# Performance work log

Measured on AMD Instinct MI355X. Metric: run time of the kernel, lower is better.

## Reference

```python
import jax, jax.numpy as jnp
import numpy as np

SIZE = (128, 160, 128)  # (D, H, W)
BATCH, CHANNELS = 4, 1


def setup_inputs() -> dict:
    key = jax.random.key(0)
    k1, k2 = jax.random.split(key)
    src = jax.random.normal(k1, (BATCH, CHANNELS) + SIZE, dtype=jnp.float32)
    # near-identity affine [B, 3, 4] so most sampled coords land in-volume
    eye = jnp.concatenate([jnp.eye(3, dtype=jnp.float32), jnp.zeros((3, 1), jnp.float32)], axis=1)
    affine_matrix = eye[None] + 0.05 * jax.random.normal(k2, (BATCH, 3, 4), dtype=jnp.float32)
    return {"src": src, "affine_matrix": affine_matrix}


def _mesh_matrix(D, H, W):
    # rows: dim0 (D), dim1 (H), dim2 (W), ones  -> [4, N]
    gz, gy, gx = jnp.meshgrid(jnp.arange(D), jnp.arange(H), jnp.arange(W), indexing='ij')
    N = D * H * W
    return jnp.stack([gz.reshape(N), gy.reshape(N), gx.reshape(N),
                      jnp.ones((N,), jnp.int32)], axis=0).astype(jnp.float32)


def _trilinear_border(src, ix, iy, iz):
    # src: [B, C, D, H, W]; ix/iy/iz: [B, N] unnormalized pixel coords (x->W, y->H, z->D)
    B, C, D, H, W = src.shape
    # border padding: clamp coordinate before interpolation (matches PyTorch)
    ix = jnp.clip(ix, 0.0, W - 1.0)
    iy = jnp.clip(iy, 0.0, H - 1.0)
    iz = jnp.clip(iz, 0.0, D - 1.0)
    x0f, y0f, z0f = jnp.floor(ix), jnp.floor(iy), jnp.floor(iz)
    wx = (ix - x0f)[:, None, :]  # [B,1,N]
    wy = (iy - y0f)[:, None, :]
    wz = (iz - z0f)[:, None, :]
    x0 = x0f.astype(jnp.int32); x1 = jnp.minimum(x0 + 1, W - 1)
    y0 = y0f.astype(jnp.int32); y1 = jnp.minimum(y0 + 1, H - 1)
    z0 = z0f.astype(jnp.int32); z1 = jnp.minimum(z0 + 1, D - 1)
    flat = src.reshape(B, C, D * H * W)
    N = ix.shape[-1]

    def gather(zz, yy, xx):
        idx = (zz * H + yy) * W + xx  # [B, N]
        idx = jnp.broadcast_to(idx[:, None, :], (B, C, N))
        return jnp.take_along_axis(flat, idx, axis=2)  # [B, C, N]

    c000 = gather(z0, y0, x0); c001 = gather(z0, y0, x1)
    c010 = gather(z0, y1, x0); c011 = gather(z0, y1, x1)
    c100 = gather(z1, y0, x0); c101 = gather(z1, y0, x1)
    c110 = gather(z1, y1, x0); c111 = gather(z1, y1, x1)
    c00 = c000 + (c001 - c000) * wx
    c01 = c010 + (c011 - c010) * wx
    c10 = c100 + (c101 - c100) * wx
    c11 = c110 + (c111 - c110) * wx
    c0 = c00 + (c01 - c00) * wy
    c1 = c10 + (c11 - c10) * wy
    return c0 + (c1 - c0) * wz  # [B, C, N]


def reference(src, affine_matrix):
    D, H, W = SIZE
    B, C = src.shape[:2]
    mesh = _mesh_matrix(D, H, W)  # [4, N]
    loc = jnp.einsum('bij,jn->bin', affine_matrix, mesh)  # [B, 3, N] voxel coords
    sizes = jnp.array([D, H, W], jnp.float32)
    g = 2.0 * (loc / (sizes[None, :, None] - 1.0) - 0.5)  # normalized, dims (d0,d1,d2)
    # flip to grid_sample (x, y, z) ordering, then unnormalize (align_corners=False)
    ix = ((g[:, 2] + 1.0) * W - 1.0) * 0.5
    iy = ((g[:, 1] + 1.0) * H - 1.0) * 0.5
    iz = ((g[:, 0] + 1.0) * D - 1.0) * 0.5
    out = _trilinear_border(src, ix, iy, iz)  # [B, C, N]
    return out.reshape(B, C, D, H, W)
```

## Files before the change

kernel.cpp:

```cpp
#include <hip/hip_runtime.h>

#define DD 128
#define HH 160
#define WW 128
#define BB 4
#define HW  20480
#define DHW 2621440

#define TX 32
#define TY 8
#define TZ 8
#define XT 4
#define YT 20
#define ZT 16
#define NWG (XT * YT * ZT * BB)
#define NXCD 8
#define CPX (NWG / NXCD)

#define FZE   14
#define FYE   14
#define PITCH 44
#define SLABF (FYE * PITCH)
#define ROWB  (PITCH * 4)
#define SLABB (SLABF * 4)
#define NIT 9
#define LDSALLOC (NIT * 1024)

typedef float f2 __attribute__((ext_vector_type(2), aligned(4)));
typedef float v2 __attribute__((ext_vector_type(2)));

__global__ __launch_bounds__(256)
void st_affine_kernel(const float* __restrict__ src,
                      const float* __restrict__ aff,
                      float* __restrict__ out) {
    __shared__ float lds[LDSALLOC];

    const int wgid = blockIdx.x;
    const int lin  = (wgid & (NXCD - 1)) * CPX + (wgid >> 3);
    const int xt = lin & 3;
    const int l2 = lin >> 2;
    const int yt = l2 % YT;
    const int l3 = l2 / YT;
    const int zt = l3 & (ZT - 1);
    const int b  = l3 >> 4;
    const int x0t = xt * TX, y0t = yt * TY, z0t = zt * TZ;

    const float* A = aff + b * 12;
    const float cD = 128.f/127.f, cH = 160.f/159.f, cW = 128.f/127.f;
    const float pz0 = A[0]*cD, pz1 = A[1]*cD, pz2 = A[2]*cD,  pz3 = fmaf(A[3],  cD, -0.5f);
    const float py0 = A[4]*cH, py1 = A[5]*cH, py2 = A[6]*cH,  py3 = fmaf(A[7],  cH, -0.5f);
    const float px0 = A[8]*cW, px1 = A[9]*cW, px2 = A[10]*cW, px3 = fmaf(A[11], cW, -0.5f);

    const float hz = (TZ - 1) * 0.5f, hy = (TY - 1) * 0.5f, hx = (TX - 1) * 0.5f;
    const float ccz = (float)z0t + hz, ccy = (float)y0t + hy, ccx = (float)x0t + hx;
    const float izcn = fmaf(pz0, ccz, fmaf(pz1, ccy, fmaf(pz2, ccx, pz3)));
    const float iycn = fmaf(py0, ccz, fmaf(py1, ccy, fmaf(py2, ccx, py3)));
    const float ixcn = fmaf(px0, ccz, fmaf(px1, ccy, fmaf(px2, ccx, px3)));
    const float rz = fmaf(fabsf(pz0), hz, fmaf(fabsf(pz1), hy, fmaf(fabsf(pz2), hx, 1e-3f)));
    const float ry = fmaf(fabsf(py0), hz, fmaf(fabsf(py1), hy, fmaf(fabsf(py2), hx, 1e-3f)));
    const float rx = fmaf(fabsf(px0), hz, fmaf(fabsf(px1), hy, fmaf(fabsf(px2), hx, 1e-3f)));
    const float mnz = izcn - rz, mxz = izcn + rz;
    const float mny = iycn - ry, mxy = iycn + ry;
    const float mnx = ixcn - rx, mxx = ixcn + rx;

    const bool interior =
        (mnz > 0.02f) && (mxz < 126.98f) &&
        (mny > 0.02f) && (mxy < 158.98f) &&
        (mnx > 0.02f) && (mxx < 126.98f);

    const int xlo = max(0, (int)floorf(__builtin_amdgcn_fmed3f(mnx, 0.f, 127.f)) - 1);
    const int ylo = max(0, (int)floorf(__builtin_amdgcn_fmed3f(mny, 0.f, 159.f)) - 1);
    const int zlo = max(0, (int)floorf(__builtin_amdgcn_fmed3f(mnz, 0.f, 127.f)) - 1);
    const int xhi = min(WW - 2, (int)floorf(__builtin_amdgcn_fmed3f(mxx, 0.f, 127.f)) + 1);
    const int yhi = min(HH - 2, (int)floorf(__builtin_amdgcn_fmed3f(mxy, 0.f, 159.f)) + 1);
    const int zhi = min(DD - 2, (int)floorf(__builtin_amdgcn_fmed3f(mxz, 0.f, 127.f)) + 1);

    const int xlo4 = xlo & ~3;
    const int XE4  = xhi - xlo4 + 2;
    const int YE   = yhi - ylo + 2;
    const int ZE   = zhi - zlo + 2;
    const bool fits = (XE4 <= PITCH) && (YE <= FYE) && (ZE <= FZE);

    const float zloF = (float)zlo, yloF = (float)ylo, xlo4F = (float)xlo4;

    const int tid  = threadIdx.x;
    const int lane = tid & 63;
    const int wid  = tid >> 6;

    const int xq = x0t + (lane & 31);
    const int yo = y0t + (lane >> 5) + (wid << 1);
    const float fx0 = (float)xq, fy = (float)yo, fzb = (float)z0t;

    const float izb0 = fmaf(pz0, fzb, fmaf(pz1, fy, fmaf(pz2, fx0, pz3)));
    const float iyb0 = fmaf(py0, fzb, fmaf(py1, fy, fmaf(py2, fx0, py3)));
    const float ixb0 = fmaf(px0, fzb, fmaf(px1, fy, fmaf(px2, fx0, px3)));

    const float* sb = src + b * DHW;
    float* dst0 = out + (size_t)(((b * DD + z0t) * HH + yo) * WW + xq);

    if (fits) {
        const float RC154 = 1.f / 154.f, RC11 = 1.f / 11.f;
        const float gbase = fmaf(zloF, 20480.f, fmaf(yloF, 128.f, xlo4F));
        const int totalCh = ZE * FYE * 11;
        const int nIt = (totalCh + 255) >> 8;
        for (int it = 0; it < nIt; ++it) {
            const int k = (it << 8) + tid;
            float kf  = (float)k;
            float zif = floorf(fmaf(kf, RC154, 0.5f * RC154));
            float rem = fmaf(zif, -154.f, kf);
            float yif = floorf(fmaf(rem, RC11, 0.5f * RC11));
            float xif = fmaf(yif, -11.f, rem);
            float gf  = fmaf(zif, 20480.f, fmaf(yif, 128.f, fmaf(xif, 4.f, gbase)));
            int g = min((int)gf, DHW - 4);
            __builtin_amdgcn_global_load_lds(
                (const __attribute__((address_space(1))) void*)(sb + g),
                (__attribute__((address_space(3))) void*)(lds + (size_t)(((it << 8) + (wid << 6)) * 4)),
                16, 0, 0);
        }
    }
    __syncthreads();

    const char* Lb = (const char*)lds;

    auto triL = [&](int o0, int o1, v2 wx, v2 wy, v2 wz) -> v2 {
        f2 a00 = *(const f2*)(Lb + o0);
        f2 a01 = *(const f2*)(Lb + o0 + ROWB);
        f2 a10 = *(const f2*)(Lb + o0 + SLABB);
        f2 a11 = *(const f2*)(Lb + o0 + SLABB + ROWB);
        f2 b00 = *(const f2*)(Lb + o1);
        f2 b01 = *(const f2*)(Lb + o1 + ROWB);
        f2 b10 = *(const f2*)(Lb + o1 + SLABB);
        f2 b11 = *(const f2*)(Lb + o1 + SLABB + ROWB);
        v2 c00 = {fmaf(a00.y - a00.x, wx.x, a00.x), fmaf(b00.y - b00.x, wx.y, b00.x)};
        v2 c01 = {fmaf(a01.y - a01.x, wx.x, a01.x), fmaf(b01.y - b01.x, wx.y, b01.x)};
        v2 c10 = {fmaf(a10.y - a10.x, wx.x, a10.x), fmaf(b10.y - b10.x, wx.y, b10.x)};
        v2 c11 = {fmaf(a11.y - a11.x, wx.x, a11.x), fmaf(b11.y - b11.x, wx.y, b11.x)};
        v2 c0 = c00 + (c01 - c00) * wy;
        v2 c1 = c10 + (c11 - c10) * wy;
        return c0 + (c1 - c0) * wz;
    };

    if (fits) {
        const v2 dzv = {2.f * pz0, 2.f * pz0};
        const v2 dyv = {2.f * py0, 2.f * py0};
        const v2 dxv = {2.f * px0, 2.f * px0};
        const float hiZ = 127.f - zloF, capZ = 126.f - zloF;
        const float hiY = 159.f - yloF, capY = 158.f - yloF;
        const float hiX = 127.f - xlo4F, capX = 126.f - xlo4F;

        v2 az = {izb0 - zloF, izb0 + pz0 - zloF};
        v2 ay = {iyb0 - yloF, iyb0 + py0 - yloF};
        v2 ax = {ixb0 - xlo4F, ixb0 + px0 - xlo4F};

#pragma unroll
        for (int s = 0; s < 4; ++s) {
            v2 cz, cy, cx, wz, wy, wx;
            if (interior) {
                cz = v2{floorf(az.x), floorf(az.y)};
                cy = v2{floorf(ay.x), floorf(ay.y)};
                cx = v2{floorf(ax.x), floorf(ax.y)};
                wz = az - cz; wy = ay - cy; wx = ax - cx;
            } else {
                v2 azc = {__builtin_amdgcn_fmed3f(az.x, 0.f, hiZ),
                          __builtin_amdgcn_fmed3f(az.y, 0.f, hiZ)};
                v2 ayc = {__builtin_amdgcn_fmed3f(ay.x, 0.f, hiY),
                          __builtin_amdgcn_fmed3f(ay.y, 0.f, hiY)};
                v2 axc = {__builtin_amdgcn_fmed3f(ax.x, 0.f, hiX),
                          __builtin_amdgcn_fmed3f(ax.y, 0.f, hiX)};
                cz = v2{fminf(floorf(azc.x), capZ), fminf(floorf(azc.y), capZ)};
                cy = v2{fminf(floorf(ayc.x), capY), fminf(floorf(ayc.y), capY)};
                cx = v2{fminf(floorf(axc.x), capX), fminf(floorf(axc.y), capX)};
                wz = azc - cz; wy = ayc - cy; wx = axc - cx;
            }
            v2 ob = (cz * (float)FYE + cy) * (float)ROWB + cx * 4.f;
            v2 r = triL((int)ob.x, (int)ob.y, wx, wy, wz);
            float* d = dst0 + (s << 1) * HW;
            __builtin_nontemporal_store(r.x, d);
            __builtin_nontemporal_store(r.y, d + HW);
            az += dzv; ay += dyv; ax += dxv;
        }
    } else {
        v2 az = {izb0, izb0 + pz0};
        v2 ay = {iyb0, iyb0 + py0};
        v2 ax = {ixb0, ixb0 + px0};
        const v2 dzv = {2.f * pz0, 2.f * pz0};
        const v2 dyv = {2.f * py0, 2.f * py0};
        const v2 dxv = {2.f * px0, 2.f * px0};
#pragma unroll
        for (int s = 0; s < 4; ++s) {
            v2 azc = {__builtin_amdgcn_fmed3f(az.x, 0.f, 127.f),
                      __builtin_amdgcn_fmed3f(az.y, 0.f, 127.f)};
            v2 ayc = {__builtin_amdgcn_fmed3f(ay.x, 0.f, 159.f),
                      __builtin_amdgcn_fmed3f(ay.y, 0.f, 159.f)};
            v2 axc = {__builtin_amdgcn_fmed3f(ax.x, 0.f, 127.f),
                      __builtin_amdgcn_fmed3f(ax.y, 0.f, 127.f)};
            v2 cz = {fminf(floorf(azc.x), 126.f), fminf(floorf(azc.y), 126.f)};
            v2 cy = {fminf(floorf(ayc.x), 158.f), fminf(floorf(ayc.y), 158.f)};
            v2 cx = {fminf(floorf(axc.x), 126.f), fminf(floorf(axc.y), 126.f)};
            v2 wz = azc - cz, wy = ayc - cy, wx = axc - cx;
            auto g1 = [&](float czs, float cys, float cxs, float wxs, float wys, float wzs) -> float {
                int o = (int)fmaf(czs, 20480.f, fmaf(cys, 128.f, cxs));
                const float* p = sb + o;
                f2 v00 = *(const f2*)(p);
                f2 v01 = *(const f2*)(p + WW);
                f2 v10 = *(const f2*)(p + HW);
                f2 v11 = *(const f2*)(p + HW + WW);
                float c00 = fmaf(v00.y - v00.x, wxs, v00.x);
                float c01 = fmaf(v01.y - v01.x, wxs, v01.x);
                float c10 = fmaf(v10.y - v10.x, wxs, v10.x);
                float c11 = fmaf(v11.y - v11.x, wxs, v11.x);
                float c0 = fmaf(c01 - c00, wys, c00);
                float c1 = fmaf(c11 - c10, wys, c10);
                return fmaf(c1 - c0, wzs, c0);
            };
            float* d = dst0 + (s << 1) * HW;
            __builtin_nontemporal_store(g1(cz.x, cy.x, cx.x, wx.x, wy.x, wz.x), d);
            __builtin_nontemporal_store(g1(cz.y, cy.y, cx.y, wx.y, wy.y, wz.y), d + HW);
            az += dzv; ay += dyv; ax += dxv;
        }
    }
}

extern "C" void kernel_launch(void* const* d_in, const int* in_sizes, int n_in,
                              void* d_out, int out_size, void* d_ws, size_t ws_size,
                              hipStream_t stream) {
    const float* src = (const float*)d_in[0];
    const float* aff = (const float*)d_in[1];
    float* out = (float*)d_out;

    st_affine_kernel<<<dim3(NWG), dim3(256), 0, stream>>>(src, aff, out);
}
```

Before: 24.94 us.

## Enlarge workgroup tile in y and tighten the LDS staging box

Changes the output tile per workgroup from 32x8x8 to 32x16x8, so each thread handles two y-rows eight apart across all eight z-slices instead of two z-slices at a time. The LDS footprint grows in y to 21 rows and the slab chunk count is adjusted to match. The conservative -1/+1 margins on the source bounding box are dropped, which shrinks the region loaded into LDS. The aim is to cut redundant halo loads relative to useful output, at the cost of more LDS per workgroup (lower occupancy), half as many workgroups, and a higher chance that tiles fall back to the slower direct-global path.

```diff
diff --git a/kernel.cpp b/kernel.cpp
--- a/kernel.cpp
+++ b/kernel.cpp
@@ -8,23 +8,22 @@
 #define DHW 2621440
 
 #define TX 32
-#define TY 8
+#define TY 16
 #define TZ 8
 #define XT 4
-#define YT 20
+#define YT 10
 #define ZT 16
 #define NWG (XT * YT * ZT * BB)
 #define NXCD 8
 #define CPX (NWG / NXCD)
 
 #define FZE   14
-#define FYE   14
+#define FYE   21
 #define PITCH 44
-#define SLABF (FYE * PITCH)
 #define ROWB  (PITCH * 4)
-#define SLABB (SLABF * 4)
-#define NIT 9
-#define LDSALLOC (NIT * 1024)
+#define SLABB (FYE * ROWB)
+#define SLABCH (FYE * 11)
+#define LDSALLOC 13312
 
 typedef float f2 __attribute__((ext_vector_type(2), aligned(4)));
 typedef float v2 __attribute__((ext_vector_type(2)));
@@ -68,12 +67,12 @@
         (mny > 0.02f) && (mxy < 158.98f) &&
         (mnx > 0.02f) && (mxx < 126.98f);
 
-    const int xlo = max(0, (int)floorf(__builtin_amdgcn_fmed3f(mnx, 0.f, 127.f)) - 1);
-    const int ylo = max(0, (int)floorf(__builtin_amdgcn_fmed3f(mny, 0.f, 159.f)) - 1);
-    const int zlo = max(0, (int)floorf(__builtin_amdgcn_fmed3f(mnz, 0.f, 127.f)) - 1);
-    const int xhi = min(WW - 2, (int)floorf(__builtin_amdgcn_fmed3f(mxx, 0.f, 127.f)) + 1);
-    const int yhi = min(HH - 2, (int)floorf(__builtin_amdgcn_fmed3f(mxy, 0.f, 159.f)) + 1);
-    const int zhi = min(DD - 2, (int)floorf(__builtin_amdgcn_fmed3f(mxz, 0.f, 127.f)) + 1);
+    const int zlo = max(0, (int)floorf(__builtin_amdgcn_fmed3f(mnz, 0.f, 127.f)));
+    const int ylo = max(0, (int)floorf(__builtin_amdgcn_fmed3f(mny, 0.f, 159.f)));
+    const int xlo = max(0, (int)floorf(__builtin_amdgcn_fmed3f(mnx, 0.f, 127.f)));
+    const int zhi = min(DD - 2, (int)floorf(__builtin_amdgcn_fmed3f(mxz, 0.f, 127.f)));
+    const int yhi = min(HH - 2, (int)floorf(__builtin_amdgcn_fmed3f(mxy, 0.f, 159.f)));
+    const int xhi = min(WW - 2, (int)floorf(__builtin_amdgcn_fmed3f(mxx, 0.f, 127.f)));
 
     const int xlo4 = xlo & ~3;
     const int XE4  = xhi - xlo4 + 2;
@@ -94,20 +93,21 @@
     const float izb0 = fmaf(pz0, fzb, fmaf(pz1, fy, fmaf(pz2, fx0, pz3)));
     const float iyb0 = fmaf(py0, fzb, fmaf(py1, fy, fmaf(py2, fx0, py3)));
     const float ixb0 = fmaf(px0, fzb, fmaf(px1, fy, fmaf(px2, fx0, px3)));
+    const float dz8 = 8.f * pz1, dy8 = 8.f * py1, dx8 = 8.f * px1;
 
     const float* sb = src + b * DHW;
     float* dst0 = out + (size_t)(((b * DD + z0t) * HH + yo) * WW + xq);
 
     if (fits) {
-        const float RC154 = 1.f / 154.f, RC11 = 1.f / 11.f;
+        const float RC231 = 1.f / 231.f, RC11 = 1.f / 11.f;
         const float gbase = fmaf(zloF, 20480.f, fmaf(yloF, 128.f, xlo4F));
-        const int totalCh = ZE * FYE * 11;
+        const int totalCh = ZE * SLABCH;
         const int nIt = (totalCh + 255) >> 8;
         for (int it = 0; it < nIt; ++it) {
             const int k = (it << 8) + tid;
             float kf  = (float)k;
-            float zif = floorf(fmaf(kf, RC154, 0.5f * RC154));
-            float rem = fmaf(zif, -154.f, kf);
+            float zif = floorf(fmaf(kf, RC231, 0.5f * RC231));
+            float rem = fmaf(zif, -231.f, kf);
             float yif = floorf(fmaf(rem, RC11, 0.5f * RC11));
             float xif = fmaf(yif, -11.f, rem);
             float gf  = fmaf(zif, 20480.f, fmaf(yif, 128.f, fmaf(xif, 4.f, gbase)));
@@ -141,19 +141,17 @@
     };
 
     if (fits) {
-        const v2 dzv = {2.f * pz0, 2.f * pz0};
-        const v2 dyv = {2.f * py0, 2.f * py0};
-        const v2 dxv = {2.f * px0, 2.f * px0};
+        const v2 dzv = {pz0, pz0}, dyv = {py0, py0}, dxv = {px0, px0};
         const float hiZ = 127.f - zloF, capZ = 126.f - zloF;
         const float hiY = 159.f - yloF, capY = 158.f - yloF;
         const float hiX = 127.f - xlo4F, capX = 126.f - xlo4F;
 
-        v2 az = {izb0 - zloF, izb0 + pz0 - zloF};
-        v2 ay = {iyb0 - yloF, iyb0 + py0 - yloF};
-        v2 ax = {ixb0 - xlo4F, ixb0 + px0 - xlo4F};
+        v2 az = {izb0 - zloF, izb0 + dz8 - zloF};
+        v2 ay = {iyb0 - yloF, iyb0 + dy8 - yloF};
+        v2 ax = {ixb0 - xlo4F, ixb0 + dx8 - xlo4F};
 
 #pragma unroll
-        for (int s = 0; s < 4; ++s) {
+        for (int s = 0; s < TZ; ++s) {
             v2 cz, cy, cx, wz, wy, wx;
             if (interior) {
                 cz = v2{floorf(az.x), floorf(az.y)};
@@ -174,20 +172,18 @@
             }
             v2 ob = (cz * (float)FYE + cy) * (float)ROWB + cx * 4.f;
             v2 r = triL((int)ob.x, (int)ob.y, wx, wy, wz);
-            float* d = dst0 + (s << 1) * HW;
+            float* d = dst0 + s * HW;
             __builtin_nontemporal_store(r.x, d);
-            __builtin_nontemporal_store(r.y, d + HW);
+            __builtin_nontemporal_store(r.y, d + 8 * WW);
             az += dzv; ay += dyv; ax += dxv;
         }
     } else {
-        v2 az = {izb0, izb0 + pz0};
-        v2 ay = {iyb0, iyb0 + py0};
-        v2 ax = {ixb0, ixb0 + px0};
-        const v2 dzv = {2.f * pz0, 2.f * pz0};
-        const v2 dyv = {2.f * py0, 2.f * py0};
-        const v2 dxv = {2.f * px0, 2.f * px0};
+        v2 az = {izb0, izb0 + dz8};
+        v2 ay = {iyb0, iyb0 + dy8};
+        v2 ax = {ixb0, ixb0 + dx8};
+        const v2 dzv = {pz0, pz0}, dyv = {py0, py0}, dxv = {px0, px0};
 #pragma unroll
-        for (int s = 0; s < 4; ++s) {
+        for (int s = 0; s < TZ; ++s) {
             v2 azc = {__builtin_amdgcn_fmed3f(az.x, 0.f, 127.f),
                       __builtin_amdgcn_fmed3f(az.y, 0.f, 127.f)};
             v2 ayc = {__builtin_amdgcn_fmed3f(ay.x, 0.f, 159.f),
@@ -213,9 +209,9 @@
                 float c1 = fmaf(c11 - c10, wys, c10);
                 return fmaf(c1 - c0, wzs, c0);
             };
-            float* d = dst0 + (s << 1) * HW;
+            float* d = dst0 + s * HW;
             __builtin_nontemporal_store(g1(cz.x, cy.x, cx.x, wx.x, wy.x, wz.x), d);
-            __builtin_nontemporal_store(g1(cz.y, cy.y, cx.y, wx.y, wy.y, wz.y), d + HW);
+            __builtin_nontemporal_store(g1(cz.y, cy.y, cx.y, wx.y, wy.y, wz.y), d + 8 * WW);
             az += dzv; ay += dyv; ax += dxv;
         }
     }
```

Result: faster. 23.85 us (-4.4%).
